# Performance work log

Hardware: AMD Instinct MI355X
Metric: run time of the kernel (lower is better)

## Reference

```python
import jax, jax.numpy as jnp
import numpy as np

N_NODES = 50000
N_EDGES = 600000
IN_DIM, HID_DIM, OUT_DIM = 128, 256, 40


def setup_inputs() -> dict:
    key = jax.random.key(0)
    ks = jax.random.split(key, 10)
    x = jax.random.normal(ks[0], (N_NODES, IN_DIM), dtype=jnp.float32)
    edge_index = jax.random.randint(ks[1], (2, N_EDGES), 0, N_NODES, dtype=jnp.int64)
    def lin(k, out_d, in_d):
        s = 1.0 / np.sqrt(in_d)
        return jax.random.uniform(k, (out_d, in_d), jnp.float32, -s, s)
    # SAGEConv: lin_l (on aggregated neighbors, with bias) + lin_r (on self, no bias)
    params = {
        "Wl1": lin(ks[2], HID_DIM, IN_DIM), "bl1": jnp.zeros((HID_DIM,), jnp.float32), "Wr1": lin(ks[3], HID_DIM, IN_DIM),
        "Wl2": lin(ks[4], HID_DIM, HID_DIM), "bl2": jnp.zeros((HID_DIM,), jnp.float32), "Wr2": lin(ks[5], HID_DIM, HID_DIM),
        "Wl3": lin(ks[6], OUT_DIM, HID_DIM), "bl3": jnp.zeros((OUT_DIM,), jnp.float32), "Wr3": lin(ks[7], OUT_DIM, HID_DIM),
    }
    return {"x": x, "edge_index": edge_index, **params}


def _sage_conv(x, src, dst, Wl, bl, Wr):
    # mean-aggregate source features into destination nodes
    n = x.shape[0]
    agg = jax.ops.segment_sum(x[src], dst, num_segments=n)          # [N, d_in]
    cnt = jax.ops.segment_sum(jnp.ones_like(dst, dtype=x.dtype), dst, num_segments=n)
    mean = agg / jnp.maximum(cnt, 1.0)[:, None]
    return mean @ Wl.T + bl + x @ Wr.T


def reference(x, edge_index, Wl1, bl1, Wr1, Wl2, bl2, Wr2, Wl3, bl3, Wr3):
    src, dst = edge_index[0], edge_index[1]
    h = _sage_conv(x, src, dst, Wl1, bl1, Wr1)
    h = jax.nn.relu(h)  # dropout is identity in eval mode
    h = _sage_conv(h, src, dst, Wl2, bl2, Wr2)
    h = jax.nn.relu(h)
    h = _sage_conv(h, src, dst, Wl3, bl3, Wr3)
    return jax.nn.log_softmax(h, axis=1)
```

## Files before the change

kernel.cpp:

```cpp
#include <hip/hip_runtime.h>
#include <hip/hip_bf16.h>

#define IN_DIM 128
#define HID_DIM 256
#define OUT_DIM 40
#define SCAN_CHUNK 2048

typedef __attribute__((ext_vector_type(8))) __bf16 bf16x8;
typedef __attribute__((ext_vector_type(4))) float f32x4;

__device__ inline ushort f2bf(float f) {
    uint u = __builtin_bit_cast(uint, f);
    u = (u + 0x7fff + ((u >> 16) & 1)) >> 16;
    return (ushort)u;
}
__device__ inline float bfl(uint u) { return __builtin_bit_cast(float, u << 16); }
__device__ inline float bfh(uint u) { return __builtin_bit_cast(float, u & 0xffff0000u); }

__device__ inline void gload_lds16(const ushort* g, ushort* l) {
    __builtin_amdgcn_global_load_lds((const __attribute__((address_space(1))) void*)g,
                                     (__attribute__((address_space(3))) void*)l, 16, 0, 0);
}

__device__ inline int xcd_swizzle(int b, int G) {
    int q = G >> 3, r = G & 7;
    int xcd = b & 7, j = b >> 3;
    return (xcd < r ? xcd * (q + 1) : r * (q + 1) + (xcd - r) * q) + j;
}

__global__ __launch_bounds__(256) void prep_kernel(
    const float* __restrict__ x, ushort* __restrict__ xb, int n4, int XB,
    const float* __restrict__ Wl1, const float* __restrict__ Wr1,
    const float* __restrict__ Wl2, const float* __restrict__ Wr2,
    const float* __restrict__ Wl3, const float* __restrict__ Wr3,
    ushort* __restrict__ o1l, ushort* __restrict__ o1r,
    ushort* __restrict__ o2l, ushort* __restrict__ o2r,
    ushort* __restrict__ o3l, ushort* __restrict__ o3r, int WB,
    const int* __restrict__ dst, int* __restrict__ cnt, int E) {
    int b = blockIdx.x;
    if (b < XB) {
        int i = b * 256 + threadIdx.x;
        if (i < n4) {
            float4 v = ((const float4*)x)[i];
            uint2 o;
            o.x = (uint)f2bf(v.x) | ((uint)f2bf(v.y) << 16);
            o.y = (uint)f2bf(v.z) | ((uint)f2bf(v.w) << 16);
            ((uint2*)xb)[i] = o;
        }
        return;
    }
    b -= XB;
    if (b < WB) {
        int idx = b * 256 + threadIdx.x;
        if (idx < 32768) {
            int j = idx & 7, ln = (idx >> 3) & 15, quad = (idx >> 7) & 3;
            int kk = (idx >> 9) & 3, ct = (idx >> 11) & 3, cb = idx >> 13;
            int o = cb * 64 + ct * 16 + ln;
            int k = kk * 32 + quad * 8 + j;
            o1l[idx] = f2bf(Wl1[o * 128 + k]);
            o1r[idx] = f2bf(Wr1[o * 128 + k]);
            return;
        }
        idx -= 32768;
        if (idx < 65536) {
            int j = idx & 7, ln = (idx >> 3) & 15, quad = (idx >> 7) & 3;
            int kk = (idx >> 9) & 7, ct = (idx >> 12) & 3, cb = idx >> 14;
            int o = cb * 64 + ct * 16 + ln;
            int k = kk * 32 + quad * 8 + j;
            o2l[idx] = f2bf(Wl2[o * 256 + k]);
            o2r[idx] = f2bf(Wr2[o * 256 + k]);
            return;
        }
        idx -= 65536;
        if (idx < 48 * 256) {
            int row = idx >> 8;
            int col = idx & 255;
            ushort vl = 0, vr = 0;
            if (row < OUT_DIM) {
                vl = f2bf(Wl3[row * 256 + col]);
                vr = f2bf(Wr3[row * 256 + col]);
            }
            o3l[idx] = vl;
            o3r[idx] = vr;
        }
        return;
    }
    b -= WB;
    int e = b * 256 + threadIdx.x;
    if (e < E) atomicAdd(&cnt[dst[e]], 1);
}

__global__ __launch_bounds__(256) void scan_pass1(const int* __restrict__ cnt,
                                                  int* __restrict__ bsum, int N) {
    __shared__ int red[256];
    const int base = blockIdx.x * SCAN_CHUNK;
    int s = 0;
    for (int i = threadIdx.x; i < SCAN_CHUNK; i += 256) {
        int idx = base + i;
        if (idx < N) s += cnt[idx];
    }
    red[threadIdx.x] = s;
    __syncthreads();
    for (int o = 128; o > 0; o >>= 1) {
        if (threadIdx.x < o) red[threadIdx.x] += red[threadIdx.x + o];
        __syncthreads();
    }
    if (threadIdx.x == 0) bsum[blockIdx.x] = red[0];
}

__global__ __launch_bounds__(256) void scan_pass3(const int* __restrict__ cnt,
                                                  const int* __restrict__ bsum,
                                                  int* __restrict__ rowptr,
                                                  int* __restrict__ cursor,
                                                  float* __restrict__ inv,
                                                  int N, int E, int SB) {
    __shared__ int ls[256];
    __shared__ int boff;
    if (threadIdx.x == 0) {
        int r = 0;
        for (int i = 0; i < blockIdx.x; ++i) r += bsum[i];
        boff = r;
    }
    const int tbase = blockIdx.x * SCAN_CHUNK + threadIdx.x * 8;
    int c[8];
    int s = 0;
#pragma unroll
    for (int j = 0; j < 8; ++j) {
        int idx = tbase + j;
        c[j] = (idx < N) ? cnt[idx] : 0;
        s += c[j];
    }
    ls[threadIdx.x] = s;
    __syncthreads();
    for (int o = 1; o < 256; o <<= 1) {
        int u = (threadIdx.x >= o) ? ls[threadIdx.x - o] : 0;
        __syncthreads();
        ls[threadIdx.x] += u;
        __syncthreads();
    }
    int run = boff + ls[threadIdx.x] - s;
#pragma unroll
    for (int j = 0; j < 8; ++j) {
        int idx = tbase + j;
        if (idx < N) {
            rowptr[idx] = run;
            cursor[idx] = run;
            inv[idx] = 1.0f / fmaxf((float)c[j], 1.0f);
            run += c[j];
        }
    }
    if (blockIdx.x == 0 && threadIdx.x == 0) rowptr[N] = E;
}

__global__ __launch_bounds__(256) void fill_kernel(const int* __restrict__ src,
                                                   const int* __restrict__ dst,
                                                   int* __restrict__ cursor,
                                                   int* __restrict__ srcs, int E) {
    int e = blockIdx.x * 256 + threadIdx.x;
    if (e < E) {
        int pos = atomicAdd(&cursor[dst[e]], 1);
        srcs[pos] = src[e];
    }
}

template <int D>
__global__ __launch_bounds__(256) void gather_mean_bf(const ushort* __restrict__ feat,
                                                      const int* __restrict__ rowptr,
                                                      const int* __restrict__ srcs,
                                                      const float* __restrict__ inv,
                                                      ushort* __restrict__ out, int N) {
    constexpr int V = D / 64;
    const int wave = threadIdx.x >> 6;
    const int lane = threadIdx.x & 63;
    const int n = blockIdx.x * 4 + wave;
    if (n >= N) return;
    const int beg = rowptr[n];
    const int end = rowptr[n + 1];
    const int col = lane * V;
    float a0 = 0.f, a1 = 0.f, a2 = 0.f, a3 = 0.f;
    int e = beg;
    if constexpr (V == 4) {
        for (; e + 7 < end; e += 8) {
            uint2 q[8];
#pragma unroll
            for (int j = 0; j < 8; ++j)
                q[j] = *(const uint2*)&feat[(long long)srcs[e + j] * D + col];
#pragma unroll
            for (int j = 0; j < 8; ++j) {
                a0 += bfl(q[j].x); a1 += bfh(q[j].x);
                a2 += bfl(q[j].y); a3 += bfh(q[j].y);
            }
        }
        for (; e + 3 < end; e += 4) {
            uint2 q[4];
#pragma unroll
            for (int j = 0; j < 4; ++j)
                q[j] = *(const uint2*)&feat[(long long)srcs[e + j] * D + col];
#pragma unroll
            for (int j = 0; j < 4; ++j) {
                a0 += bfl(q[j].x); a1 += bfh(q[j].x);
                a2 += bfl(q[j].y); a3 += bfh(q[j].y);
            }
        }
        for (; e < end; ++e) {
            uint2 q0 = *(const uint2*)&feat[(long long)srcs[e] * D + col];
            a0 += bfl(q0.x); a1 += bfh(q0.x); a2 += bfl(q0.y); a3 += bfh(q0.y);
        }
        const float sc = inv[n];
        uint2 o;
        o.x = (uint)f2bf(a0 * sc) | ((uint)f2bf(a1 * sc) << 16);
        o.y = (uint)f2bf(a2 * sc) | ((uint)f2bf(a3 * sc) << 16);
        *(uint2*)&out[(long long)n * D + col] = o;
    } else {
        for (; e + 7 < end; e += 8) {
            uint q[8];
#pragma unroll
            for (int j = 0; j < 8; ++j)
                q[j] = *(const uint*)&feat[(long long)srcs[e + j] * D + col];
#pragma unroll
            for (int j = 0; j < 8; ++j) {
                a0 += bfl(q[j]); a1 += bfh(q[j]);
            }
        }
        for (; e + 3 < end; e += 4) {
            uint q[4];
#pragma unroll
            for (int j = 0; j < 4; ++j)
                q[j] = *(const uint*)&feat[(long long)srcs[e + j] * D + col];
#pragma unroll
            for (int j = 0; j < 4; ++j) {
                a0 += bfl(q[j]); a1 += bfh(q[j]);
            }
        }
        for (; e < end; ++e) {
            uint q0 = *(const uint*)&feat[(long long)srcs[e] * D + col];
            a0 += bfl(q0); a1 += bfh(q0);
        }
        const float sc = inv[n];
        uint o = (uint)f2bf(a0 * sc) | ((uint)f2bf(a1 * sc) << 16);
        *(uint*)&out[(long long)n * D + col] = o;
    }
}

template <int K, bool RELU, bool OUTBF>
__global__ __launch_bounds__(512, 4) void sage_gemm_mfma(const ushort* __restrict__ Amean,
                                                         const ushort* __restrict__ Aself,
                                                         const ushort* __restrict__ Wl,
                                                         const float* __restrict__ bias,
                                                         const ushort* __restrict__ Wr,
                                                         void* __restrict__ outv, int N, int O,
                                                         int G) {
    constexpr int NK = K / 32;
    constexpr int TILE = 64 * K;
    constexpr int CHUNKS = TILE / 512;
    __shared__ __align__(16) ushort Ws[2 * TILE];

    const int tid = threadIdx.x;
    const int wave = tid >> 6;
    const int lane = tid & 63;
    const int ln = lane & 15;
    const int quad = lane >> 4;

    const int wid = xcd_swizzle(blockIdx.x, G);
    const int cb = wid & 3;
    const int bm0 = (wid >> 2) * 256;

    {
        const ushort* gl = Wl + (size_t)cb * TILE;
        const ushort* gr = Wr + (size_t)cb * TILE;
#pragma unroll
        for (int c = wave; c < CHUNKS; c += 8) {
            gload_lds16(gl + c * 512 + lane * 8, &Ws[c * 512]);
            gload_lds16(gr + c * 512 + lane * 8, &Ws[TILE + c * 512]);
        }
    }

    int arow[2];
#pragma unroll
    for (int rt = 0; rt < 2; ++rt) {
        int r = bm0 + wave * 32 + rt * 16 + ln;
        arow[rt] = min(r, N - 1);
    }

    bf16x8 areg[NK][2];
#pragma unroll
    for (int kk = 0; kk < NK; ++kk)
#pragma unroll
        for (int rt = 0; rt < 2; ++rt)
            areg[kk][rt] = *(const bf16x8*)&Amean[(long long)arow[rt] * K + kk * 32 + quad * 8];

    f32x4 acc[2][4] = {};
    __syncthreads();

#pragma unroll
    for (int kk = 0; kk < NK; ++kk) {
#pragma unroll
        for (int ct = 0; ct < 4; ++ct) {
            bf16x8 b = *(const bf16x8*)&Ws[((ct * NK + kk) * 64 + lane) * 8];
#pragma unroll
            for (int rt = 0; rt < 2; ++rt)
                acc[rt][ct] = __builtin_amdgcn_mfma_f32_16x16x32_bf16(areg[kk][rt], b, acc[rt][ct], 0, 0, 0);
        }
#pragma unroll
        for (int rt = 0; rt < 2; ++rt)
            areg[kk][rt] = *(const bf16x8*)&Aself[(long long)arow[rt] * K + kk * 32 + quad * 8];
    }

#pragma unroll
    for (int kk = 0; kk < NK; ++kk) {
#pragma unroll
        for (int ct = 0; ct < 4; ++ct) {
            bf16x8 b = *(const bf16x8*)&Ws[TILE + ((ct * NK + kk) * 64 + lane) * 8];
#pragma unroll
            for (int rt = 0; rt < 2; ++rt)
                acc[rt][ct] = __builtin_amdgcn_mfma_f32_16x16x32_bf16(areg[kk][rt], b, acc[rt][ct], 0, 0, 0);
        }
    }

#pragma unroll
    for (int rt = 0; rt < 2; ++rt) {
        int rbase = bm0 + wave * 32 + rt * 16 + quad * 4;
#pragma unroll
        for (int ct = 0; ct < 4; ++ct) {
            int col = cb * 64 + ct * 16 + ln;
            if (col >= O) continue;
            float bv = bias[col];
#pragma unroll
            for (int r = 0; r < 4; ++r) {
                int row = rbase + r;
                if (row >= N) continue;
                float v = acc[rt][ct][r] + bv;
                if (RELU) v = fmaxf(v, 0.f);
                if (OUTBF)
                    ((ushort*)outv)[(long long)row * O + col] = f2bf(v);
                else
                    ((float*)outv)[(long long)row * O + col] = v;
            }
        }
    }
}

template <int K>
__global__ __launch_bounds__(256, 3) void sage_gemm_pre(const ushort* __restrict__ A0,
                                                        const ushort* __restrict__ Wl,
                                                        const ushort* __restrict__ Wr,
                                                        ushort* __restrict__ P,
                                                        float* __restrict__ S, int N, int O) {
    constexpr int KP = 2 * K + 8;
    constexpr int NK = K / 32;
    __shared__ __align__(16) ushort Ws[48 * KP];

    const int tid = threadIdx.x;
    const int wave = tid >> 6;
    const int lane = tid & 63;
    const int ln = lane & 15;
    const int quad = lane >> 4;
    const int bm0 = blockIdx.x * 64;

    const int arow = min(bm0 + wave * 16 + ln, N - 1);

#pragma unroll
    for (int i = tid; i < 48 * (K / 8); i += 256) {
        int row = i / (K / 8);
        int c8 = (i % (K / 8)) * 8;
        *(ulonglong2*)&Ws[row * KP + c8] =
            *(const ulonglong2*)&Wl[(long long)row * K + c8];
        *(ulonglong2*)&Ws[row * KP + K + c8] =
            *(const ulonglong2*)&Wr[(long long)row * K + c8];
    }
    __syncthreads();

#pragma unroll
    for (int phase = 0; phase < 2; ++phase) {
        f32x4 acc[3] = {};
#pragma unroll
        for (int kk = 0; kk < NK; ++kk) {
            bf16x8 a = *(const bf16x8*)&A0[(long long)arow * K + kk * 32 + quad * 8];
#pragma unroll
            for (int ct = 0; ct < 3; ++ct) {
                bf16x8 b = *(const bf16x8*)&Ws[(ct * 16 + ln) * KP + phase * K + kk * 32 + quad * 8];
                acc[ct] = __builtin_amdgcn_mfma_f32_16x16x32_bf16(a, b, acc[ct], 0, 0, 0);
            }
        }
        int rbase = bm0 + wave * 16 + quad * 4;
#pragma unroll
        for (int ct = 0; ct < 3; ++ct) {
            int col = ct * 16 + ln;
            if (col >= O) continue;
#pragma unroll
            for (int r = 0; r < 4; ++r) {
                int row = rbase + r;
                if (row >= N) continue;
                if (phase == 0)
                    P[(long long)row * O + col] = f2bf(acc[ct][r]);
                else
                    S[(long long)row * O + col] = acc[ct][r];
            }
        }
    }
}

__global__ __launch_bounds__(256) void agg_bias_lsm(const ushort* __restrict__ P,
                                                    const float* __restrict__ S,
                                                    const float* __restrict__ bias,
                                                    const int* __restrict__ rowptr,
                                                    const int* __restrict__ srcs,
                                                    const float* __restrict__ inv,
                                                    float* __restrict__ out, int N) {
    const int wave = threadIdx.x >> 6;
    const int lane = threadIdx.x & 63;
    const int n = blockIdx.x * 4 + wave;
    if (n >= N) return;
    const int beg = rowptr[n];
    const int end = rowptr[n + 1];
    const bool act = lane < OUT_DIM;
    const int cidx = act ? lane : 0;

    float acc = 0.f;
    int e = beg;
    for (; e + 3 < end; e += 4) {
        int s0 = srcs[e], s1 = srcs[e + 1], s2 = srcs[e + 2], s3 = srcs[e + 3];
        float v0 = __builtin_bit_cast(float, (uint)P[(long long)s0 * OUT_DIM + cidx] << 16);
        float v1 = __builtin_bit_cast(float, (uint)P[(long long)s1 * OUT_DIM + cidx] << 16);
        float v2 = __builtin_bit_cast(float, (uint)P[(long long)s2 * OUT_DIM + cidx] << 16);
        float v3 = __builtin_bit_cast(float, (uint)P[(long long)s3 * OUT_DIM + cidx] << 16);
        acc += (v0 + v1) + (v2 + v3);
    }
    for (; e < end; ++e)
        acc += __builtin_bit_cast(float, (uint)P[(long long)srcs[e] * OUT_DIM + cidx] << 16);

    float v = act ? (acc * inv[n] + S[(long long)n * OUT_DIM + lane] + bias[lane]) : -INFINITY;
    float m = v;
#pragma unroll
    for (int o = 32; o > 0; o >>= 1) m = fmaxf(m, __shfl_xor(m, o, 64));
    float ex = act ? expf(v - m) : 0.f;
    float sm = ex;
#pragma unroll
    for (int o = 32; o > 0; o >>= 1) sm += __shfl_xor(sm, o, 64);
    float ls = logf(sm);
    if (act) out[(long long)n * OUT_DIM + lane] = v - m - ls;
}

extern "C" void kernel_launch(void* const* d_in, const int* in_sizes, int n_in,
                              void* d_out, int out_size, void* d_ws, size_t ws_size,
                              hipStream_t stream) {
    const float* x   = (const float*)d_in[0];
    const int*   ei  = (const int*)d_in[1];
    const float* Wl1 = (const float*)d_in[2];
    const float* bl1 = (const float*)d_in[3];
    const float* Wr1 = (const float*)d_in[4];
    const float* Wl2 = (const float*)d_in[5];
    const float* bl2 = (const float*)d_in[6];
    const float* Wr2 = (const float*)d_in[7];
    const float* Wl3 = (const float*)d_in[8];
    const float* bl3 = (const float*)d_in[9];
    const float* Wr3 = (const float*)d_in[10];
    float* out = (float*)d_out;

    const int N = in_sizes[0] / IN_DIM;
    const int E = in_sizes[1] / 2;
    const int* src = ei;
    const int* dst = ei + E;

    char* w = (char*)d_ws;
    size_t off = 0;
    auto alloc = [&](size_t bytes) {
        void* p = w + off;
        off = (off + bytes + 255) & ~(size_t)255;
        return p;
    };
    ushort* xb   = (ushort*)alloc((size_t)N * IN_DIM * 2);
    ushort* M    = (ushort*)alloc((size_t)N * HID_DIM * 2);
    ushort* H1   = (ushort*)alloc((size_t)N * HID_DIM * 2);
    ushort* H2   = (ushort*)alloc((size_t)N * HID_DIM * 2);
    ushort* P3   = (ushort*)alloc((size_t)N * OUT_DIM * 2);
    float*  S3   = (float*)alloc((size_t)N * OUT_DIM * 4);
    float*  inv  = (float*)alloc((size_t)N * 4);
    int*    cnt  = (int*)alloc((size_t)N * 4);
    int*    rowptr = (int*)alloc((size_t)(N + 1) * 4);
    int*    cursor = (int*)alloc((size_t)N * 4);
    int*    srcs = (int*)alloc((size_t)E * 4);
    int*    bsum = (int*)alloc(256 * 4);
    ushort* Wl1b = (ushort*)alloc(256 * 128 * 2);
    ushort* Wr1b = (ushort*)alloc(256 * 128 * 2);
    ushort* Wl2b = (ushort*)alloc(256 * 256 * 2);
    ushort* Wr2b = (ushort*)alloc(256 * 256 * 2);
    ushort* Wl3b = (ushort*)alloc(48 * 256 * 2);
    ushort* Wr3b = (ushort*)alloc(48 * 256 * 2);

    const int n4 = N * IN_DIM / 4;
    const int XB = (n4 + 255) / 256;
    const int WB = (32768 + 65536 + 48 * 256 + 255) / 256;
    const int HB = (E + 255) / 256;
    hipMemsetAsync(cnt, 0, (size_t)N * sizeof(int), stream);
    prep_kernel<<<XB + WB + HB, 256, 0, stream>>>(
        x, xb, n4, XB,
        Wl1, Wr1, Wl2, Wr2, Wl3, Wr3,
        Wl1b, Wr1b, Wl2b, Wr2b, Wl3b, Wr3b, WB,
        dst, cnt, E);

    const int SB = (N + SCAN_CHUNK - 1) / SCAN_CHUNK;
    scan_pass1<<<SB, 256, 0, stream>>>(cnt, bsum, N);
    scan_pass3<<<SB, 256, 0, stream>>>(cnt, bsum, rowptr, cursor, inv, N, E, SB);
    fill_kernel<<<HB, 256, 0, stream>>>(src, dst, cursor, srcs, E);

    const int gm = (N + 255) / 256;
    const int G = 4 * gm;
    const int gg = (N + 3) / 4;

    gather_mean_bf<IN_DIM><<<gg, 256, 0, stream>>>(xb, rowptr, srcs, inv, M, N);
    sage_gemm_mfma<IN_DIM, true, true><<<G, 512, 0, stream>>>(
        M, xb, Wl1b, bl1, Wr1b, H1, N, HID_DIM, G);

    gather_mean_bf<HID_DIM><<<gg, 256, 0, stream>>>(H1, rowptr, srcs, inv, M, N);
    sage_gemm_mfma<HID_DIM, true, true><<<G, 512, 0, stream>>>(
        M, H1, Wl2b, bl2, Wr2b, H2, N, HID_DIM, G);

    sage_gemm_pre<HID_DIM><<<(N + 63) / 64, 256, 0, stream>>>(
        H2, Wl3b, Wr3b, P3, S3, N, OUT_DIM);
    agg_bias_lsm<<<gg, 256, 0, stream>>>(P3, S3, bl3, rowptr, srcs, inv, out, N);
}
```

Baseline: 350.7 us.

## Pack multiple nodes per wave in gather-mean with 16-byte loads

The mean-aggregation kernel now has each lane load 8 bf16 values (16 bytes) per neighbour row. A wave therefore covers 4 nodes at D=128 or 2 nodes at D=256, where before one wave handled one node. This uses wider memory transactions and processes more nodes per block, with grid sizes adjusted to match. The cost is divergence inside a wave, since the packed nodes have different degrees and lanes idle until the longest neighbour list finishes.

```diff
diff --git a/kernel.cpp b/kernel.cpp
--- a/kernel.cpp
+++ b/kernel.cpp
@@ -169,76 +169,50 @@
                                                       const int* __restrict__ srcs,
                                                       const float* __restrict__ inv,
                                                       ushort* __restrict__ out, int N) {
-    constexpr int V = D / 64;
+    constexpr int LPN = D / 8;
+    constexpr int NPW = 64 / LPN;
+    constexpr int NPB = 4 * NPW;
     const int wave = threadIdx.x >> 6;
     const int lane = threadIdx.x & 63;
-    const int n = blockIdx.x * 4 + wave;
-    if (n >= N) return;
-    const int beg = rowptr[n];
-    const int end = rowptr[n + 1];
-    const int col = lane * V;
+    const int sub = lane / LPN;
+    const int sl = lane % LPN;
+    const int n = blockIdx.x * NPB + wave * NPW + sub;
+    const bool alive = n < N;
+    const int beg = alive ? rowptr[n] : 0;
+    const int end = alive ? rowptr[n + 1] : 0;
+    const int col = sl * 8;
+
     float a0 = 0.f, a1 = 0.f, a2 = 0.f, a3 = 0.f;
+    float a4 = 0.f, a5 = 0.f, a6 = 0.f, a7 = 0.f;
     int e = beg;
-    if constexpr (V == 4) {
-        for (; e + 7 < end; e += 8) {
-            uint2 q[8];
-#pragma unroll
-            for (int j = 0; j < 8; ++j)
-                q[j] = *(const uint2*)&feat[(long long)srcs[e + j] * D + col];
-#pragma unroll
-            for (int j = 0; j < 8; ++j) {
-                a0 += bfl(q[j].x); a1 += bfh(q[j].x);
-                a2 += bfl(q[j].y); a3 += bfh(q[j].y);
-            }
-        }
-        for (; e + 3 < end; e += 4) {
-            uint2 q[4];
-#pragma unroll
-            for (int j = 0; j < 4; ++j)
-                q[j] = *(const uint2*)&feat[(long long)srcs[e + j] * D + col];
-#pragma unroll
-            for (int j = 0; j < 4; ++j) {
-                a0 += bfl(q[j].x); a1 += bfh(q[j].x);
-                a2 += bfl(q[j].y); a3 += bfh(q[j].y);
-            }
-        }
-        for (; e < end; ++e) {
-            uint2 q0 = *(const uint2*)&feat[(long long)srcs[e] * D + col];
-            a0 += bfl(q0.x); a1 += bfh(q0.x); a2 += bfl(q0.y); a3 += bfh(q0.y);
-        }
+    for (; e + 3 < end; e += 4) {
+        uint4 q[4];
+#pragma unroll
+        for (int j = 0; j < 4; ++j)
+            q[j] = *(const uint4*)&feat[(long long)srcs[e + j] * D + col];
+#pragma unroll
+        for (int j = 0; j < 4; ++j) {
+            a0 += bfl(q[j].x); a1 += bfh(q[j].x);
+            a2 += bfl(q[j].y); a3 += bfh(q[j].y);
+            a4 += bfl(q[j].z); a5 += bfh(q[j].z);
+            a6 += bfl(q[j].w); a7 += bfh(q[j].w);
+        }
+    }
+    for (; e < end; ++e) {
+        uint4 q = *(const uint4*)&feat[(long long)srcs[e] * D + col];
+        a0 += bfl(q.x); a1 += bfh(q.x);
+        a2 += bfl(q.y); a3 += bfh(q.y);
+        a4 += bfl(q.z); a5 += bfh(q.z);
+        a6 += bfl(q.w); a7 += bfh(q.w);
+    }
+    if (alive) {
         const float sc = inv[n];
-        uint2 o;
+        uint4 o;
         o.x = (uint)f2bf(a0 * sc) | ((uint)f2bf(a1 * sc) << 16);
         o.y = (uint)f2bf(a2 * sc) | ((uint)f2bf(a3 * sc) << 16);
-        *(uint2*)&out[(long long)n * D + col] = o;
-    } else {
-        for (; e + 7 < end; e += 8) {
-            uint q[8];
-#pragma unroll
-            for (int j = 0; j < 8; ++j)
-                q[j] = *(const uint*)&feat[(long long)srcs[e + j] * D + col];
-#pragma unroll
-            for (int j = 0; j < 8; ++j) {
-                a0 += bfl(q[j]); a1 += bfh(q[j]);
-            }
-        }
-        for (; e + 3 < end; e += 4) {
-            uint q[4];
-#pragma unroll
-            for (int j = 0; j < 4; ++j)
-                q[j] = *(const uint*)&feat[(long long)srcs[e + j] * D + col];
-#pragma unroll
-            for (int j = 0; j < 4; ++j) {
-                a0 += bfl(q[j]); a1 += bfh(q[j]);
-            }
-        }
-        for (; e < end; ++e) {
-            uint q0 = *(const uint*)&feat[(long long)srcs[e] * D + col];
-            a0 += bfl(q0); a1 += bfh(q0);
-        }
-        const float sc = inv[n];
-        uint o = (uint)f2bf(a0 * sc) | ((uint)f2bf(a1 * sc) << 16);
-        *(uint*)&out[(long long)n * D + col] = o;
+        o.z = (uint)f2bf(a4 * sc) | ((uint)f2bf(a5 * sc) << 16);
+        o.w = (uint)f2bf(a6 * sc) | ((uint)f2bf(a7 * sc) << 16);
+        *(uint4*)&out[(long long)n * D + col] = o;
     }
 }
 
@@ -506,13 +480,15 @@
 
     const int gm = (N + 255) / 256;
     const int G = 4 * gm;
+    const int gg128 = (N + 15) / 16;
+    const int gg256 = (N + 7) / 8;
     const int gg = (N + 3) / 4;
 
-    gather_mean_bf<IN_DIM><<<gg, 256, 0, stream>>>(xb, rowptr, srcs, inv, M, N);
+    gather_mean_bf<IN_DIM><<<gg128, 256, 0, stream>>>(xb, rowptr, srcs, inv, M, N);
     sage_gemm_mfma<IN_DIM, true, true><<<G, 512, 0, stream>>>(
         M, xb, Wl1b, bl1, Wr1b, H1, N, HID_DIM, G);
 
-    gather_mean_bf<HID_DIM><<<gg, 256, 0, stream>>>(H1, rowptr, srcs, inv, M, N);
+    gather_mean_bf<HID_DIM><<<gg256, 256, 0, stream>>>(H1, rowptr, srcs, inv, M, N);
     sage_gemm_mfma<HID_DIM, true, true><<<G, 512, 0, stream>>>(
         M, H1, Wl2b, bl2, Wr2b, H2, N, HID_DIM, G);
 
```

Result: no change. 344.3 us (-1.8%).
